# Kernel optimization log

Measured on AMD Instinct MI355X. Metric: run time of the kernel, lower is better.

The kernel has to match this reference:

```python
import jax, jax.numpy as jnp
import numpy as np

R = 80   # volume_reso
B, NV, C, H, W = 1, 4, 32, 64, 64


def _voxel_grid():
    line = np.linspace(-1.0, 1.0, R)
    x, y, z = np.meshgrid(line, line, line, indexing='ij')
    return jnp.asarray(np.stack([x, y, z]).reshape(3, -1), dtype=jnp.float32)  # (3, R^3)


def grid_sample_pix(img, coords):
    """Bilinear sample at pixel coords (align_corners=True convention, zero padding).
    img: (BN, C, H, W); coords: (BN, N, 2) as (x, y) in pixel units.
    Returns vals (BN, C, N) and in-bounds mask (BN, N)."""
    BN, Cc, Hh, Ww = img.shape
    x, y = coords[..., 0], coords[..., 1]
    mask = ((x >= 0) & (x <= Ww - 1) & (y >= 0) & (y <= Hh - 1)).astype(img.dtype)
    x0 = jnp.floor(x); y0 = jnp.floor(y)
    x1 = x0 + 1.0;     y1 = y0 + 1.0
    wx1 = x - x0; wx0 = 1.0 - wx1
    wy1 = y - y0; wy0 = 1.0 - wy1
    imgf = img.reshape(BN, Cc, Hh * Ww)

    def corner(xi, yi, w):
        valid = ((xi >= 0) & (xi <= Ww - 1) & (yi >= 0) & (yi <= Hh - 1)).astype(img.dtype)
        xc = jnp.clip(xi, 0, Ww - 1).astype(jnp.int32)
        yc = jnp.clip(yi, 0, Hh - 1).astype(jnp.int32)
        flat = yc * Ww + xc                                   # (BN, N)
        vals = jnp.take_along_axis(imgf, flat[:, None, :], axis=2)  # (BN, C, N)
        return vals * (valid * w)[:, None, :]

    out = (corner(x0, y0, wx0 * wy0) + corner(x1, y0, wx1 * wy0)
           + corner(x0, y1, wx0 * wy1) + corner(x1, y1, wx1 * wy1))
    return out, mask


def setup_inputs() -> dict:
    key = jax.random.key(0)
    ks = jax.random.split(key, 7)
    feats = jax.random.normal(ks[0], (B, NV, C, H, W), dtype=jnp.float32)
    # structured pinhole projection matrices (K @ w2c embedded in 4x4)
    f = 55.0; cx = (W - 1) / 2.0; cy = (H - 1) / 2.0
    poses = np.zeros((B, NV, 4, 4), np.float32)
    for v in range(NV):
        poses[0, v] = np.array([[f, 0, cx, 0.0],
                                [0, f, cy, 0.1 * v],
                                [0, 0, 1.0, 3.0 + 0.2 * v],
                                [0, 0, 0, 1.0]], np.float32)
    return {
        'feats': feats,
        'source_poses': jnp.asarray(poses),
        'W1': jax.random.normal(ks[1], (32, 32), jnp.float32) / np.sqrt(32.0),
        'b1': jax.random.normal(ks[2], (32,), jnp.float32) * 0.01,
        'W2': jax.random.normal(ks[3], (32, 16), jnp.float32) / np.sqrt(32.0),
        'b2': jax.random.normal(ks[4], (16,), jnp.float32) * 0.01,
        'W3': jax.random.normal(ks[5], (16, 8), jnp.float32) / np.sqrt(16.0),
        'b3': jax.random.normal(ks[6], (8,), jnp.float32) * 0.01,
    }


def reference(feats, source_poses, W1, b1, W2, b2, W3, b3):
    N = R ** 3
    xyz = _voxel_grid()                                             # (3, N)
    homo = jnp.concatenate([xyz, jnp.ones((1, N), xyz.dtype)], 0)   # (4, N)
    proj = jnp.einsum('bvij,jn->bvin', source_poses, homo)[:, :, :3]  # (B,NV,3,N)
    z = proj[:, :, 2]                                               # (B,NV,N)
    mask_valid_depth = (z > 0).astype(feats.dtype)
    uv = proj[:, :, :2] / proj[:, :, 2:3]                           # (B,NV,2,N)
    coords = jnp.transpose(uv, (0, 1, 3, 2)).reshape(B * NV, N, 2)
    vals, mask = grid_sample_pix(feats.reshape(B * NV, C, H, W), coords)
    vf = jnp.transpose(vals.reshape(B, NV, C, N), (0, 1, 3, 2))     # (B,NV,N,C)
    mask = mask.reshape(B, NV, N) * mask_valid_depth                # (B,NV,N)
    weight = mask / (jnp.sum(mask, axis=1, keepdims=True) + 1e-8)
    # small MLP 32 -> 32 -> 16 -> 8
    h = jax.nn.relu(vf @ W1 + b1)
    h = jax.nn.relu(h @ W2 + b2)
    h = h @ W3 + b3                                                 # (B,NV,N,8)
    w = weight[..., None]
    mean = jnp.sum(h * w, axis=1, keepdims=True)                    # (B,1,N,8)
    var = jnp.sum(w * (h - mean) ** 2, axis=1)                      # (B,N,8)
    mv = jnp.concatenate([mean[:, 0], var], axis=-1)                # (B,N,16)
    vol = mv.reshape(B, R, R, R, 16)                                # (B,X,Y,Z,16)
    return jnp.transpose(vol, (0, 4, 3, 2, 1))                      # (B,16,Z,Y,X)
```

## Files before the change

kernel.cpp:

```cpp
#include <hip/hip_runtime.h>
#include <cstddef>

#define RR 80
#define NVIEW 4
#define CH 32
#define IH 64
#define IW 64
#define NPIX (IH*IW)
#define NVOX (RR*RR*RR)

#define PLANE_H (NPIX*8)
#define VIEW_H  (4*PLANE_H)

typedef _Float16 half4_t  __attribute__((ext_vector_type(4)));
typedef _Float16 half8_t  __attribute__((ext_vector_type(8)));
typedef float    float4_t __attribute__((ext_vector_type(4)));

#define H2T_STRIDE 20

__global__ __launch_bounds__(256) void g_precompute(
    const float* __restrict__ feats, const float* __restrict__ W1,
    _Float16* __restrict__ G)
{
    int g = blockIdx.x >> 6;
    int p = (blockIdx.x & 63)*256 + threadIdx.x;
    __shared__ float sW1[CH*8];
    if (threadIdx.x < CH*8) {
        int ic = threadIdx.x >> 3, e = threadIdx.x & 7;
        sW1[threadIdx.x] = W1[ic*CH + 8*g + e];
    }
    __syncthreads();
    int v  = p >> 12;
    int yx = p & 4095;
    const float* fb = feats + ((size_t)v*CH)*NPIX + yx;
    float acc[8];
    #pragma unroll
    for (int e=0;e<8;++e) acc[e] = 0.f;
    #pragma unroll
    for (int ic=0; ic<CH; ++ic) {
        float fv = fb[(size_t)ic*NPIX];
        #pragma unroll
        for (int e=0;e<8;++e) acc[e] = fmaf(fv, sW1[ic*8+e], acc[e]);
    }
    half8_t h;
    #pragma unroll
    for (int e=0;e<8;++e) h[e] = (_Float16)acc[e];
    *(half8_t*)(G + (size_t)v*VIEW_H + (size_t)g*PLANE_H + (size_t)yx*8) = h;
}

__global__ __launch_bounds__(256) void dgfv_main(
    const _Float16* __restrict__ G,
    const float* __restrict__ poses,
    const float* __restrict__ b1,
    const float* __restrict__ W2, const float* __restrict__ b2,
    const float* __restrict__ W3, const float* __restrict__ b3,
    float* __restrict__ out)
{
    __shared__ __align__(16) _Float16 h1buf[4][64*40];
    __shared__ __align__(16) float    mkbuf[4][64];
    __shared__ __align__(16) _Float16 h2t[4][16*H2T_STRIDE];

    const int wid  = threadIdx.x >> 6;
    const int lane = threadIdx.x & 63;
    const int lq   = lane >> 4;
    const int lc   = lane & 15;
    const int voxBase = blockIdx.x*256 + wid*64;
    const int vox  = voxBase + lane;

    half8_t w2f;
    #pragma unroll
    for (int j=0;j<8;++j) w2f[j] = (_Float16)W2[(lq*8+j)*16 + lc];
    half4_t w3f;
    #pragma unroll
    for (int j=0;j<4;++j) w3f[j] = (lc<8) ? (_Float16)W3[(lq*4+j)*8 + lc]
                                          : (_Float16)0.f;
    const float b2c = b2[lc];
    const float b3c = (lc<8) ? b3[lc] : 0.f;
    const float4_t c1init = {b2c,b2c,b2c,b2c};
    const float4_t c2init = {b3c,b3c,b3c,b3c};

    half8_t b1h[4];
    #pragma unroll
    for (int g=0;g<4;++g) {
        #pragma unroll
        for (int e=0;e<8;++e) b1h[g][e] = (_Float16)b1[8*g+e];
    }

    int i   = vox % RR;
    int rem = vox / RR;
    int j_  = rem % RR;
    int k_  = rem / RR;
    const float step = 2.0f/(float)(RR-1);
    float x = fmaf((float)i,  step, -1.0f);
    float y = fmaf((float)j_, step, -1.0f);
    float z = fmaf((float)k_, step, -1.0f);

    float accA[16], accB[16], accM[16];
    #pragma unroll
    for (int q=0;q<16;++q) { accA[q]=0.f; accB[q]=0.f; accM[q]=0.f; }

    for (int v = 0; v < NVIEW; ++v) {
        const float* P = poses + v*16;
        float px = fmaf(P[0],x, fmaf(P[1],y, fmaf(P[2], z, P[3])));
        float py = fmaf(P[4],x, fmaf(P[5],y, fmaf(P[6], z, P[7])));
        float pz = fmaf(P[8],x, fmaf(P[9],y, fmaf(P[10],z, P[11])));
        float u  = px/pz;
        float w  = py/pz;

        float mk = (pz > 0.f && u >= 0.f && u <= (float)(IW-1)
                              && w >= 0.f && w <= (float)(IH-1)) ? 1.f : 0.f;

        float fx0 = floorf(u), fy0 = floorf(w);
        float tx = u - fx0, ty = w - fy0;
        bool bx0 = (fx0 >=  0.f) && (fx0 <= (float)(IW-1));
        bool bx1 = (fx0 >= -1.f) && (fx0 <= (float)(IW-2));
        bool by0 = (fy0 >=  0.f) && (fy0 <= (float)(IH-1));
        bool by1 = (fy0 >= -1.f) && (fy0 <= (float)(IH-2));
        int x0 = (int)fminf(fmaxf(fx0,      0.f), (float)(IW-1));
        int x1 = (int)fminf(fmaxf(fx0+1.f,  0.f), (float)(IW-1));
        int y0 = (int)fminf(fmaxf(fy0,      0.f), (float)(IH-1));
        int y1 = (int)fminf(fmaxf(fy0+1.f,  0.f), (float)(IH-1));

        float w00 = (bx0&&by0) ? (1.f-tx)*(1.f-ty) : 0.f;
        float w10 = (bx1&&by0) ? tx*(1.f-ty)       : 0.f;
        float w01 = (bx0&&by1) ? (1.f-tx)*ty       : 0.f;
        float w11 = (bx1&&by1) ? tx*ty             : 0.f;

        _Float16 w00h = (_Float16)w00, w10h = (_Float16)w10;
        _Float16 w01h = (_Float16)w01, w11h = (_Float16)w11;

        const _Float16* gv = G + (size_t)v*VIEW_H;
        int o00 = (y0*IW + x0)*8;
        int o10 = (y0*IW + x1)*8;
        int o01 = (y1*IW + x0)*8;
        int o11 = (y1*IW + x1)*8;

        _Float16* rowp = &h1buf[wid][lane*40];
        #pragma unroll
        for (int g=0;g<4;++g) {
            const _Float16* pl = gv + (size_t)g*PLANE_H;
            half8_t a = *(const half8_t*)(pl + o00);
            half8_t b = *(const half8_t*)(pl + o10);
            half8_t c = *(const half8_t*)(pl + o01);
            half8_t d = *(const half8_t*)(pl + o11);
            half8_t r = a*w00h + b*w10h + c*w01h + d*w11h + b1h[g];
            r = __builtin_elementwise_max(r, (half8_t)(_Float16)0.f);
            ((half8_t*)rowp)[g] = r;
        }
        mkbuf[wid][lane] = mk;
        __builtin_amdgcn_wave_barrier();

        #pragma unroll
        for (int b=0;b<4;++b) {
            half8_t a1 = *(const half8_t*)&h1buf[wid][(16*b+lc)*40 + lq*8];
            float4_t d1 = __builtin_amdgcn_mfma_f32_16x16x32_f16(a1, w2f, c1init, 0,0,0);
            #pragma unroll
            for (int r=0;r<4;++r)
                h2t[wid][(4*lq+r)*H2T_STRIDE + lc] = (_Float16)fmaxf(d1[r], 0.f);
            __builtin_amdgcn_wave_barrier();
            half4_t a2 = *(const half4_t*)&h2t[wid][lc*H2T_STRIDE + lq*4];
            float4_t d2 = __builtin_amdgcn_mfma_f32_16x16x16f16(a2, w3f, c2init, 0,0,0);
            float4 mkv = *(const float4*)&mkbuf[wid][16*b + lq*4];
            #pragma unroll
            for (int r=0;r<4;++r) {
                float h3 = d2[r];
                float m  = (r==0)?mkv.x:(r==1)?mkv.y:(r==2)?mkv.z:mkv.w;
                int idx = 4*b + r;
                accA[idx] = fmaf(m, h3,    accA[idx]);
                accB[idx] = fmaf(m, h3*h3, accB[idx]);
                accM[idx] += m;
            }
            __builtin_amdgcn_wave_barrier();
        }
        __builtin_amdgcn_wave_barrier();
    }

    float* fb = (float*)&h1buf[wid][0];
    if (lc < 8) {
        #pragma unroll
        for (int b=0;b<4;++b) {
            #pragma unroll
            for (int r=0;r<4;++r) {
                int idx  = 4*b + r;
                int voxr = 16*b + 4*lq + r;
                float S   = accM[idx] + 1e-8f;
                float inv = 1.f/S;
                float sw  = accM[idx]*inv;
                float mean= accA[idx]*inv;
                float var = fmaf(-mean*mean, (2.f - sw), accB[idx]*inv);
                fb[voxr*17 + lc]     = mean;
                fb[voxr*17 + 8 + lc] = var;
            }
        }
    }
    __builtin_amdgcn_wave_barrier();
    #pragma unroll
    for (int c=0;c<16;++c)
        out[(size_t)c*NVOX + vox] = fb[lane*17 + c];
}

extern "C" void kernel_launch(void* const* d_in, const int* in_sizes, int n_in,
                              void* d_out, int out_size, void* d_ws, size_t ws_size,
                              hipStream_t stream)
{
    const float* feats = (const float*)d_in[0];
    const float* poses = (const float*)d_in[1];
    const float* W1    = (const float*)d_in[2];
    const float* b1    = (const float*)d_in[3];
    const float* W2    = (const float*)d_in[4];
    const float* b2    = (const float*)d_in[5];
    const float* W3    = (const float*)d_in[6];
    const float* b3    = (const float*)d_in[7];
    float* out = (float*)d_out;

    _Float16* G = (_Float16*)d_ws;
    g_precompute<<<256, 256, 0, stream>>>(feats, W1, G);
    dgfv_main<<<NVOX/256, 256, 0, stream>>>(G, poses, b1, W2, b2, W3, b3, out);
}
```

Baseline: 110.5 us.

## Keep MLP in registers by transposing MFMA operands, removing LDS staging

The main kernel now assigns each lane a channel group (lq) and 16-voxel column, so each lane gathers only one 8-channel plane per voxel instead of all four. The MFMA calls are transposed (weights as A, activations as B), so the layer outputs land directly in the next MFMA's operand layout. This removes the shared-memory buffers, the wave barriers and the final LDS transpose for the output write. Projection math is now repeated per lane group (four times per voxel), and the division is replaced by rcp plus one Newton step, which can change rounding slightly.

```diff
diff --git a/kernel.cpp b/kernel.cpp
--- a/kernel.cpp
+++ b/kernel.cpp
@@ -15,8 +15,6 @@
 typedef _Float16 half4_t  __attribute__((ext_vector_type(4)));
 typedef _Float16 half8_t  __attribute__((ext_vector_type(8)));
 typedef float    float4_t __attribute__((ext_vector_type(4)));
-
-#define H2T_STRIDE 20
 
 __global__ __launch_bounds__(256) void g_precompute(
     const float* __restrict__ feats, const float* __restrict__ W1,
@@ -56,147 +54,124 @@
     const float* __restrict__ W3, const float* __restrict__ b3,
     float* __restrict__ out)
 {
-    __shared__ __align__(16) _Float16 h1buf[4][64*40];
-    __shared__ __align__(16) float    mkbuf[4][64];
-    __shared__ __align__(16) _Float16 h2t[4][16*H2T_STRIDE];
-
     const int wid  = threadIdx.x >> 6;
     const int lane = threadIdx.x & 63;
     const int lq   = lane >> 4;
     const int lc   = lane & 15;
-    const int voxBase = blockIdx.x*256 + wid*64;
-    const int vox  = voxBase + lane;
+    const int vbase = blockIdx.x*256 + wid*64 + lc;
 
-    half8_t w2f;
+    half8_t w2a;
     #pragma unroll
-    for (int j=0;j<8;++j) w2f[j] = (_Float16)W2[(lq*8+j)*16 + lc];
-    half4_t w3f;
+    for (int j=0;j<8;++j) w2a[j] = (_Float16)W2[(lq*8+j)*16 + lc];
+    half4_t w3a;
     #pragma unroll
-    for (int j=0;j<4;++j) w3f[j] = (lc<8) ? (_Float16)W3[(lq*4+j)*8 + lc]
-                                          : (_Float16)0.f;
-    const float b2c = b2[lc];
-    const float b3c = (lc<8) ? b3[lc] : 0.f;
-    const float4_t c1init = {b2c,b2c,b2c,b2c};
-    const float4_t c2init = {b3c,b3c,b3c,b3c};
+    for (int j=0;j<4;++j) w3a[j] = (_Float16)W3[(lq*4+j)*8 + (lc&7)];
+    float4_t c1init, c2init;
+    #pragma unroll
+    for (int r=0;r<4;++r) {
+        c1init[r] = b2[lq*4+r];
+        c2init[r] = b3[(lq*4+r)&7];
+    }
+    half8_t b1h;
+    #pragma unroll
+    for (int j=0;j<8;++j) b1h[j] = (_Float16)b1[8*lq+j];
 
-    half8_t b1h[4];
+    const float step = 2.0f/(float)(RR-1);
+    float xs[4], ys[4], zs[4];
     #pragma unroll
-    for (int g=0;g<4;++g) {
-        #pragma unroll
-        for (int e=0;e<8;++e) b1h[g][e] = (_Float16)b1[8*g+e];
+    for (int p=0;p<4;++p) {
+        int vx = vbase + 16*p;
+        int i  = vx % RR;
+        int t  = vx / RR;
+        int j_ = t % RR;
+        int k_ = t / RR;
+        xs[p] = fmaf((float)i,  step, -1.0f);
+        ys[p] = fmaf((float)j_, step, -1.0f);
+        zs[p] = fmaf((float)k_, step, -1.0f);
     }
 
-    int i   = vox % RR;
-    int rem = vox / RR;
-    int j_  = rem % RR;
-    int k_  = rem / RR;
-    const float step = 2.0f/(float)(RR-1);
-    float x = fmaf((float)i,  step, -1.0f);
-    float y = fmaf((float)j_, step, -1.0f);
-    float z = fmaf((float)k_, step, -1.0f);
-
-    float accA[16], accB[16], accM[16];
+    float accA[16], accB[16], accM[4];
     #pragma unroll
-    for (int q=0;q<16;++q) { accA[q]=0.f; accB[q]=0.f; accM[q]=0.f; }
+    for (int q=0;q<16;++q) { accA[q]=0.f; accB[q]=0.f; }
+    #pragma unroll
+    for (int p=0;p<4;++p) accM[p]=0.f;
 
     for (int v = 0; v < NVIEW; ++v) {
         const float* P = poses + v*16;
-        float px = fmaf(P[0],x, fmaf(P[1],y, fmaf(P[2], z, P[3])));
-        float py = fmaf(P[4],x, fmaf(P[5],y, fmaf(P[6], z, P[7])));
-        float pz = fmaf(P[8],x, fmaf(P[9],y, fmaf(P[10],z, P[11])));
-        float u  = px/pz;
-        float w  = py/pz;
-
-        float mk = (pz > 0.f && u >= 0.f && u <= (float)(IW-1)
-                              && w >= 0.f && w <= (float)(IH-1)) ? 1.f : 0.f;
-
-        float fx0 = floorf(u), fy0 = floorf(w);
-        float tx = u - fx0, ty = w - fy0;
-        bool bx0 = (fx0 >=  0.f) && (fx0 <= (float)(IW-1));
-        bool bx1 = (fx0 >= -1.f) && (fx0 <= (float)(IW-2));
-        bool by0 = (fy0 >=  0.f) && (fy0 <= (float)(IH-1));
-        bool by1 = (fy0 >= -1.f) && (fy0 <= (float)(IH-2));
-        int x0 = (int)fminf(fmaxf(fx0,      0.f), (float)(IW-1));
-        int x1 = (int)fminf(fmaxf(fx0+1.f,  0.f), (float)(IW-1));
-        int y0 = (int)fminf(fmaxf(fy0,      0.f), (float)(IH-1));
-        int y1 = (int)fminf(fmaxf(fy0+1.f,  0.f), (float)(IH-1));
-
-        float w00 = (bx0&&by0) ? (1.f-tx)*(1.f-ty) : 0.f;
-        float w10 = (bx1&&by0) ? tx*(1.f-ty)       : 0.f;
-        float w01 = (bx0&&by1) ? (1.f-tx)*ty       : 0.f;
-        float w11 = (bx1&&by1) ? tx*ty             : 0.f;
-
-        _Float16 w00h = (_Float16)w00, w10h = (_Float16)w10;
-        _Float16 w01h = (_Float16)w01, w11h = (_Float16)w11;
-
-        const _Float16* gv = G + (size_t)v*VIEW_H;
-        int o00 = (y0*IW + x0)*8;
-        int o10 = (y0*IW + x1)*8;
-        int o01 = (y1*IW + x0)*8;
-        int o11 = (y1*IW + x1)*8;
-
-        _Float16* rowp = &h1buf[wid][lane*40];
-        #pragma unroll
-        for (int g=0;g<4;++g) {
-            const _Float16* pl = gv + (size_t)g*PLANE_H;
-            half8_t a = *(const half8_t*)(pl + o00);
-            half8_t b = *(const half8_t*)(pl + o10);
-            half8_t c = *(const half8_t*)(pl + o01);
-            half8_t d = *(const half8_t*)(pl + o11);
-            half8_t r = a*w00h + b*w10h + c*w01h + d*w11h + b1h[g];
-            r = __builtin_elementwise_max(r, (half8_t)(_Float16)0.f);
-            ((half8_t*)rowp)[g] = r;
-        }
-        mkbuf[wid][lane] = mk;
-        __builtin_amdgcn_wave_barrier();
+        const _Float16* pl = G + (size_t)v*VIEW_H + (size_t)lq*PLANE_H;
 
         #pragma unroll
-        for (int b=0;b<4;++b) {
-            half8_t a1 = *(const half8_t*)&h1buf[wid][(16*b+lc)*40 + lq*8];
-            float4_t d1 = __builtin_amdgcn_mfma_f32_16x16x32_f16(a1, w2f, c1init, 0,0,0);
+        for (int p=0;p<4;++p) {
+            float x = xs[p], y = ys[p], z = zs[p];
+            float px = fmaf(P[0],x, fmaf(P[1],y, fmaf(P[2], z, P[3])));
+            float py = fmaf(P[4],x, fmaf(P[5],y, fmaf(P[6], z, P[7])));
+            float pz = fmaf(P[8],x, fmaf(P[9],y, fmaf(P[10],z, P[11])));
+            float r0 = __builtin_amdgcn_rcpf(pz);
+            r0 = r0*(2.0f - pz*r0);
+            float u  = px*r0;
+            float w  = py*r0;
+
+            float mk = (pz > 0.f && u >= 0.f && u <= (float)(IW-1)
+                                  && w >= 0.f && w <= (float)(IH-1)) ? 1.f : 0.f;
+
+            float fx0 = floorf(u), fy0 = floorf(w);
+            float tx = u - fx0, ty = w - fy0;
+            bool bx0 = (fx0 >=  0.f) && (fx0 <= (float)(IW-1));
+            bool bx1 = (fx0 >= -1.f) && (fx0 <= (float)(IW-2));
+            bool by0 = (fy0 >=  0.f) && (fy0 <= (float)(IH-1));
+            bool by1 = (fy0 >= -1.f) && (fy0 <= (float)(IH-2));
+            int x0 = (int)fminf(fmaxf(fx0,      0.f), (float)(IW-1));
+            int x1 = (int)fminf(fmaxf(fx0+1.f,  0.f), (float)(IW-1));
+            int y0 = (int)fminf(fmaxf(fy0,      0.f), (float)(IH-1));
+            int y1 = (int)fminf(fmaxf(fy0+1.f,  0.f), (float)(IH-1));
+
+            float w00 = (bx0&&by0) ? (1.f-tx)*(1.f-ty) : 0.f;
+            float w10 = (bx1&&by0) ? tx*(1.f-ty)       : 0.f;
+            float w01 = (bx0&&by1) ? (1.f-tx)*ty       : 0.f;
+            float w11 = (bx1&&by1) ? tx*ty             : 0.f;
+
+            _Float16 w00h = (_Float16)w00, w10h = (_Float16)w10;
+            _Float16 w01h = (_Float16)w01, w11h = (_Float16)w11;
+
+            half8_t a = *(const half8_t*)(pl + (y0*IW + x0)*8);
+            half8_t b = *(const half8_t*)(pl + (y0*IW + x1)*8);
+            half8_t c = *(const half8_t*)(pl + (y1*IW + x0)*8);
+            half8_t d = *(const half8_t*)(pl + (y1*IW + x1)*8);
+            half8_t h1 = a*w00h + b*w10h + c*w01h + d*w11h + b1h;
+            h1 = __builtin_elementwise_max(h1, (half8_t)(_Float16)0.f);
+
+            float4_t d1 = __builtin_amdgcn_mfma_f32_16x16x32_f16(w2a, h1, c1init, 0,0,0);
+            half4_t h2;
             #pragma unroll
-            for (int r=0;r<4;++r)
-                h2t[wid][(4*lq+r)*H2T_STRIDE + lc] = (_Float16)fmaxf(d1[r], 0.f);
-            __builtin_amdgcn_wave_barrier();
-            half4_t a2 = *(const half4_t*)&h2t[wid][lc*H2T_STRIDE + lq*4];
-            float4_t d2 = __builtin_amdgcn_mfma_f32_16x16x16f16(a2, w3f, c2init, 0,0,0);
-            float4 mkv = *(const float4*)&mkbuf[wid][16*b + lq*4];
+            for (int r=0;r<4;++r) h2[r] = (_Float16)fmaxf(d1[r], 0.f);
+
+            float4_t d2 = __builtin_amdgcn_mfma_f32_16x16x16f16(w3a, h2, c2init, 0,0,0);
+
             #pragma unroll
             for (int r=0;r<4;++r) {
                 float h3 = d2[r];
-                float m  = (r==0)?mkv.x:(r==1)?mkv.y:(r==2)?mkv.z:mkv.w;
-                int idx = 4*b + r;
-                accA[idx] = fmaf(m, h3,    accA[idx]);
-                accB[idx] = fmaf(m, h3*h3, accB[idx]);
-                accM[idx] += m;
+                float t  = mk*h3;
+                accA[4*p+r] += t;
+                accB[4*p+r] = fmaf(t, h3, accB[4*p+r]);
             }
-            __builtin_amdgcn_wave_barrier();
+            accM[p] += mk;
         }
-        __builtin_amdgcn_wave_barrier();
     }
 
-    float* fb = (float*)&h1buf[wid][0];
-    if (lc < 8) {
+    #pragma unroll
+    for (int p=0;p<4;++p) {
+        float S   = accM[p] + 1e-8f;
+        float inv = 1.f/S;
+        float sw  = accM[p]*inv;
         #pragma unroll
-        for (int b=0;b<4;++b) {
-            #pragma unroll
-            for (int r=0;r<4;++r) {
-                int idx  = 4*b + r;
-                int voxr = 16*b + 4*lq + r;
-                float S   = accM[idx] + 1e-8f;
-                float inv = 1.f/S;
-                float sw  = accM[idx]*inv;
-                float mean= accA[idx]*inv;
-                float var = fmaf(-mean*mean, (2.f - sw), accB[idx]*inv);
-                fb[voxr*17 + lc]     = mean;
-                fb[voxr*17 + 8 + lc] = var;
-            }
+        for (int r=0;r<4;++r) {
+            float mean = accA[4*p+r]*inv;
+            float var  = fmaf(-mean*mean, (2.f - sw), accB[4*p+r]*inv);
+            float val  = (lq < 2) ? mean : var;
+            int   cch  = 4*lq + r;
+            out[(size_t)cch*NVOX + vbase + 16*p] = val;
         }
     }
-    __builtin_amdgcn_wave_barrier();
-    #pragma unroll
-    for (int c=0;c<16;++c)
-        out[(size_t)c*NVOX + vox] = fb[lane*17 + c];
 }
 
 extern "C" void kernel_launch(void* const* d_in, const int* in_sizes, int n_in,
```

Result: no change. 110.7 us (+0.2%).
